# Performance work log

Measured on AMD Instinct MI355X. Metric: run time of the kernel, lower is better.

Reference implementation:

```python
import jax, jax.numpy as jnp
import numpy as np

IN_C = 256
OUT_C = 256
KS = 3
PAD = 1
EPS = 1e-5
BLOCK_SIZE = 256  # largest power of 2 dividing IN_C
NUM_BLOCKS = IN_C // BLOCK_SIZE


def golay_sequence(n):
    pow2 = 1
    while pow2 < n:
        pow2 *= 2
    a = np.array([1.0], dtype=np.float32)
    b = np.array([1.0], dtype=np.float32)
    while len(a) < pow2:
        a, b = np.concatenate([a, b]), np.concatenate([a, -b])
    return a[:n]


def fwht(x):
    """Unnormalized fast Walsh-Hadamard transform over the last axis (Sylvester order)."""
    base = x.shape[:-1]
    n = x.shape[-1]
    h = 1
    while h < n:
        y = x.reshape(base + (n // (2 * h), 2, h))
        a, c = y[..., 0, :], y[..., 1, :]
        x = jnp.stack([a + c, a - c], axis=-2).reshape(base + (n,))
        h *= 2
    return x


def setup_inputs() -> dict:
    key = jax.random.key(0)
    k1, k2, k3 = jax.random.split(key, 3)
    x = jax.random.normal(k1, (32, IN_C, 56, 56), dtype=jnp.float32)
    fan_in = IN_C * KS * KS
    W = jax.random.normal(k2, (OUT_C, IN_C, KS, KS), dtype=jnp.float32) / np.sqrt(fan_in)
    b = jax.random.normal(k3, (OUT_C,), dtype=jnp.float32) * 0.01
    rms_w = jnp.ones((IN_C,), dtype=jnp.float32)
    return {"x": x, "W": W, "b": b, "rms_w": rms_w}


def reference(x, W, b, rms_w):
    n, c, h, w = x.shape
    golay = jnp.asarray(golay_sequence(c)).reshape(1, c, 1, 1)
    x = x * golay                                    # Golay elementwise multiply
    x = jnp.transpose(x, (0, 2, 3, 1))               # NCHW -> NHWC
    x = x.reshape(n, h, w, NUM_BLOCKS, BLOCK_SIZE)
    x = fwht(x)                                      # blockwise Hadamard butterfly
    x = x.reshape(n, h, w, c)
    # RMSNorm over channel dim
    x = x * jax.lax.rsqrt(jnp.mean(x * x, axis=-1, keepdims=True) + EPS) * rms_w
    x = jnp.transpose(x, (0, 3, 1, 2))               # NHWC -> NCHW
    out = jax.lax.conv_general_dilated(
        x, W, window_strides=(1, 1), padding=((PAD, PAD), (PAD, PAD)),
        dimension_numbers=("NCHW", "OIHW", "NCHW"))
    return out + b[None, :, None, None]
```

## Files before the change

kernel.cpp:

```cpp
#include <hip/hip_runtime.h>
#include <hip/hip_bf16.h>

typedef short v8s __attribute__((ext_vector_type(8)));
typedef float v4f __attribute__((ext_vector_type(4)));
typedef float v16f __attribute__((ext_vector_type(16)));
typedef unsigned short u16;

#define PROW 58
#define PCOL 64

static constexpr size_t A_CC_STRIDE = (size_t)32 * PROW * PCOL * 32;
static constexpr size_t A_BYTES     = 8 * A_CC_STRIDE * 2;
static constexpr size_t WB_ELEMS    = (size_t)9 * 8 * 256 * 32;

__device__ __forceinline__ void gl2lds16(const void* gptr, void* lptr) {
  auto g = (const __attribute__((address_space(1))) unsigned int*)gptr;
  auto l = (__attribute__((address_space(3))) unsigned int*)lptr;
  __builtin_amdgcn_global_load_lds(g, l, 16, 0, 0);
}

__device__ __forceinline__ u16 f2bf(float f) {
  __hip_bfloat16 h = __float2bfloat16(f);
  union { __hip_bfloat16 b; u16 u; } cv; cv.b = h; return cv.u;
}

#define WAITVM(K) asm volatile("s_waitcnt vmcnt(" #K ")" ::: "memory")

struct alignas(16) HgTab {
  u16 v[16 * 8 * 64 * 8];
  constexpr HgTab() : v{} {
    for (int ks = 0; ks < 16; ks++)
      for (int nt = 0; nt < 8; nt++)
        for (int l = 0; l < 64; l++)
          for (int j = 0; j < 8; j++) {
            int c  = ks * 16 + ((l >> 5) << 3) + j;
            int cp = (nt << 5) + (l & 31);
            int s  = (__builtin_popcount((unsigned)(c & cp)) +
                      __builtin_popcount((unsigned)(c & (c >> 1)))) & 1;
            v[(((ks << 3) + nt) << 9) + (l << 3) + j] = (u16)(s ? 0xBF80 : 0x3F80);
          }
  }
};
static_assert(sizeof(HgTab) == 131072, "HgTab size");
__device__ const HgTab HG{};

__global__ __launch_bounds__(256, 4) void fwht_kernel(
    const float* __restrict__ x, const float* __restrict__ rms_w,
    u16* __restrict__ A)
{
  __shared__ __align__(16) float xs4[4][16][64];
  __shared__ float ssbuf[2][64];

  const int tid = threadIdx.x;
  const int y = blockIdx.x;
  const int n = blockIdx.y;

  const int lane = tid & 63;
  const int wv   = tid >> 6;
  const int mt   = wv & 1;
  const int nh   = wv >> 1;
  const int l31  = lane & 31;
  const int h    = lane >> 5;

  const int pos  = mt * 32 + l31;
  const int posl = pos > 55 ? 55 : pos;

  const float* xrow = x + (size_t)n * 802816 + (size_t)y * 56;
  const int rr4 = lane >> 4;
  int c4 = (lane & 15) * 4; if (c4 > 52) c4 = 52;

#define FSTG(KS) gl2lds16(xrow + (size_t)((KS) * 16 + wv * 4 + rr4) * 3136 + c4, \
                          &xs4[(KS) & 3][wv * 4 + rr4][(lane & 15) * 4])

  v8s bfr[2][4];
#define LOADB(KS, BK) { _Pragma("unroll") for (int nt = 0; nt < 4; nt++) \
    bfr[BK][nt] = *(const v8s*)(HG.v + ((size_t)((((KS) * 8) + nh * 4 + nt) * 64 + lane)) * 8); }

  v16f acc[4];
  #pragma unroll
  for (int nt = 0; nt < 4; nt++)
    #pragma unroll
    for (int e = 0; e < 16; e++)
      acc[nt][e] = 0.0f;

  FSTG(0);
  LOADB(0, 0)
  FSTG(1);
  FSTG(2);

#define FCOMP(S) { const float* cb = &xs4[(S) & 3][0][0]; v8s ah, al; \
    _Pragma("unroll") for (int j = 0; j < 8; j++) { \
      float v = cb[(h * 8 + j) * 64 + posl]; \
      unsigned u = __float_as_uint(v); \
      unsigned hu = u & 0xFFFF0000u; \
      float r = v - __uint_as_float(hu); \
      ah[j] = (short)(hu >> 16); \
      al[j] = (short)f2bf(r); } \
    _Pragma("unroll") for (int nt = 0; nt < 4; nt++) { \
      acc[nt] = __builtin_amdgcn_mfma_f32_32x32x16_bf16(ah, bfr[(S) & 1][nt], acc[nt], 0, 0, 0); \
      acc[nt] = __builtin_amdgcn_mfma_f32_32x32x16_bf16(al, bfr[(S) & 1][nt], acc[nt], 0, 0, 0); } }

#define FSTEP(S, KV) { \
    if ((S) < 15) LOADB((S) + 1, ((S) + 1) & 1) \
    __builtin_amdgcn_sched_barrier(0); \
    WAITVM(KV); \
    __builtin_amdgcn_sched_barrier(0); \
    __builtin_amdgcn_s_barrier(); \
    if ((S) + 3 <= 15) { FSTG((S) + 3); } \
    __builtin_amdgcn_sched_barrier(0); \
    FCOMP(S) }

  FSTEP(0, 6)  FSTEP(1, 5)  FSTEP(2, 5)  FSTEP(3, 5)
  FSTEP(4, 5)  FSTEP(5, 5)  FSTEP(6, 5)  FSTEP(7, 5)
  FSTEP(8, 5)  FSTEP(9, 5)  FSTEP(10, 5) FSTEP(11, 5)
  FSTEP(12, 5) FSTEP(13, 5) FSTEP(14, 4) FSTEP(15, 0)

  #pragma unroll
  for (int g = 0; g < 16; g++) {
    float s = acc[0][g] * acc[0][g] + acc[1][g] * acc[1][g]
            + acc[2][g] * acc[2][g] + acc[3][g] * acc[3][g];
    #pragma unroll
    for (int m = 1; m <= 16; m <<= 1) s += __shfl_xor(s, m, 64);
    if (l31 == 0)
      ssbuf[nh][mt * 32 + (g & 3) + 8 * (g >> 2) + 4 * h] = s;
  }
  __syncthreads();

  float rwv[4];
  #pragma unroll
  for (int nt = 0; nt < 4; nt++)
    rwv[nt] = rms_w[nh * 128 + nt * 32 + l31];

  const int jj  = lane & 7;
  const int icq = l31 >> 3;

  #pragma unroll
  for (int g = 0; g < 16; g++) {
    const int rg   = (g & 3) + 8 * (g >> 2) + 4 * h;
    const int posg = mt * 32 + rg;
    float ssum = ssbuf[0][posg] + ssbuf[1][posg];
    float sc = rsqrtf(ssum * (1.0f / 256.0f) + 1e-5f);
    if (posg < 56) {
      const int col = posg + 1;
      const size_t rowoff = ((size_t)icq * 64 + col) * 8 + jj;
      #pragma unroll
      for (int nt = 0; nt < 4; nt++) {
        const int cc = nh * 4 + nt;
        size_t go = (((size_t)cc * 32 + n) * PROW + (y + 1)) * 2048 + rowoff;
        A[go] = f2bf(acc[nt][g] * sc * rwv[nt]);
      }
    }
  }

  {
    const v8s z = {0,0,0,0,0,0,0,0};
    int cc = tid >> 5;
    int s  = tid & 31;
    int q  = s >> 3, cidx = s & 7;
    int col = (cidx == 0) ? 0 : (56 + cidx);
    size_t rb = (((size_t)cc * 32 + n) * PROW + (y + 1)) * 2048;
    *(v8s*)(A + rb + ((size_t)q * 64 + col) * 8) = z;
  }
  if (y == 0 || y == 55) {
    const v8s z = {0,0,0,0,0,0,0,0};
    const int r = (y == 0) ? 0 : 57;
    #pragma unroll
    for (int i = 0; i < 8; i++) {
      int c = tid + 256 * i;
      int cc = c >> 8, rem = c & 255;
      size_t go = (((size_t)cc * 32 + n) * PROW + r) * 2048 + rem * 8;
      *(v8s*)(A + go) = z;
    }
  }
#undef FSTG
#undef LOADB
#undef FCOMP
#undef FSTEP
}

__global__ __launch_bounds__(256) void wconv_kernel(
    const float* __restrict__ Wf, u16* __restrict__ Wb)
{
  int t = blockIdx.x * 256 + threadIdx.x;
  int kk = t >> 16;
  int cc = (t >> 13) & 7;
  int r  = t & 8191;
  int ocb = r >> 12;
  int q   = (r >> 10) & 3;
  int ocl = (r >> 3) & 127;
  int j   = r & 7;
  int oc = ocb * 128 + ocl;
  int ic = cc * 32 + q * 8 + j;
  int ky = kk / 3, kx = kk - ky * 3;
  float w = Wf[((oc * 256 + ic) * 3 + ky) * 3 + kx];
  Wb[t] = f2bf(w);
}

__global__ __launch_bounds__(256, 4) void conv_kernel(
    const u16* __restrict__ A, const u16* __restrict__ Wb,
    const float* __restrict__ bias, float* __restrict__ out)
{
  __shared__ __align__(16) u16 As2[2][8192];

  const int tid  = threadIdx.x;
  const int lane = tid & 63;
  const int wv   = tid >> 6;
  const int wm   = wv & 1;
  const int wn   = wv >> 1;
  const int m31  = lane & 31;
  const int kh8  = lane >> 5;

  const int ocb = blockIdx.x;
  const int y0  = blockIdx.y * 2;
  const int n   = blockIdx.z;

  const u16* gA = A + ((size_t)n * PROW + y0) * 2048;

  v16f acc[2][2];
  #pragma unroll
  for (int i = 0; i < 2; i++)
    #pragma unroll
    for (int j = 0; j < 2; j++)
      #pragma unroll
      for (int e = 0; e < 16; e++)
        acc[i][j][e] = 0.0f;

  int ub[2][2];
  #pragma unroll
  for (int nf = 0; nf < 2; nf++)
    #pragma unroll
    for (int kh = 0; kh < 2; kh++) {
      int ocl = wn * 64 + nf * 32 + m31;
      int q = kh * 2 + kh8;
      ub[nf][kh] = (q * 128 + ocl) * 8;
    }

#define STAGE_A(CCV) { const u16* g = gA + (size_t)(CCV) * A_CC_STRIDE + tid * 8; \
    u16* d = &As2[(CCV) & 1][0] + tid * 8; \
    _Pragma("unroll") for (int k = 0; k < 4; k++) gl2lds16(g + k * 2048, d + k * 2048); }

#define CONV_CC(CC) { \
    WAITVM(0); \
    __builtin_amdgcn_s_barrier(); \
    if ((CC) < 7) STAGE_A((CC) + 1) \
    __builtin_amdgcn_sched_barrier(0); \
    { const u16* asb = &As2[(CC) & 1][0]; \
      _Pragma("unroll") for (int ky = 0; ky < 3; ky++) \
        _Pragma("unroll") for (int kx = 0; kx < 3; kx++) { \
          const u16* bt = Wb + (size_t)((((ky * 3 + kx) * 8 + (CC)) * 8192) + ocb * 4096); \
          v8s bf[2][2]; \
          _Pragma("unroll") for (int nf = 0; nf < 2; nf++) \
            _Pragma("unroll") for (int kh = 0; kh < 2; kh++) \
              bf[nf][kh] = *(const v8s*)(bt + ub[nf][kh]); \
          v8s af[2][2]; \
          _Pragma("unroll") for (int mf = 0; mf < 2; mf++) \
            _Pragma("unroll") for (int kh = 0; kh < 2; kh++) { \
              int col = mf * 32 + m31 + kx; \
              col = col > 63 ? 63 : col; \
              int q = kh * 2 + kh8; \
              af[mf][kh] = *(const v8s*)(asb + ((wm + ky) * 4 + q) * 512 + col * 8); } \
          _Pragma("unroll") for (int mf = 0; mf < 2; mf++) \
            _Pragma("unroll") for (int nf = 0; nf < 2; nf++) { \
              acc[mf][nf] = __builtin_amdgcn_mfma_f32_32x32x16_bf16(af[mf][0], bf[nf][0], acc[mf][nf], 0, 0, 0); \
              acc[mf][nf] = __builtin_amdgcn_mfma_f32_32x32x16_bf16(af[mf][1], bf[nf][1], acc[mf][nf], 0, 0, 0); } \
        } } }

  STAGE_A(0)

  CONV_CC(0) CONV_CC(1) CONV_CC(2) CONV_CC(3)
  CONV_CC(4) CONV_CC(5) CONV_CC(6) CONV_CC(7)

#undef STAGE_A
#undef CONV_CC

  const int yrow = y0 + wm;
  #pragma unroll
  for (int nf = 0; nf < 2; nf++) {
    const int oc = ocb * 128 + wn * 64 + nf * 32 + m31;
    const float bb = bias[oc];
    float* orow = out + ((size_t)(n * 256 + oc) * 56 + yrow) * 56;
    #pragma unroll
    for (int mf = 0; mf < 2; mf++) {
      #pragma unroll
      for (int g = 0; g < 4; g++) {
        const int x0 = mf * 32 + 8 * g + 4 * kh8;
        if (x0 < 56) {
          v4f val = { acc[mf][nf][4*g+0] + bb, acc[mf][nf][4*g+1] + bb,
                      acc[mf][nf][4*g+2] + bb, acc[mf][nf][4*g+3] + bb };
          *(v4f*)(orow + x0) = val;
        }
      }
    }
  }
}

extern "C" void kernel_launch(void* const* d_in, const int* in_sizes, int n_in,
                              void* d_out, int out_size, void* d_ws, size_t ws_size,
                              hipStream_t stream)
{
  const float* x     = (const float*)d_in[0];
  const float* Wf    = (const float*)d_in[1];
  const float* bias  = (const float*)d_in[2];
  const float* rms_w = (const float*)d_in[3];
  float* out = (float*)d_out;

  if (ws_size < A_BYTES + WB_ELEMS * 2) return;

  u16* Abf = (u16*)d_ws;
  u16* Wb  = (u16*)((char*)d_ws + A_BYTES);

  fwht_kernel<<<dim3(56, 32), 256, 0, stream>>>(x, rms_w, Abf);
  wconv_kernel<<<dim3((int)(WB_ELEMS / 256)), 256, 0, stream>>>(Wf, Wb);
  conv_kernel<<<dim3(2, 28, 32), 256, 0, stream>>>(Abf, Wb, bias, out);
}
```

Before: 333.1 us.

## Software-pipeline weight fragment loads across ky rows and swizzle block order

Weight (B) fragments for each ky row are now prefetched into registers, in a ping-pong buffer, one ky step ahead, including the next channel chunk's first row. This hides global-load latency behind the MFMAs instead of stalling on each load. The vmcnt wait is relaxed from 0 to 12 so these loads can stay in flight. The grid is flattened to 1D and swizzled so the two output-channel blocks of nearby row pairs run together, which should improve L2 reuse of activations. The larger register footprint forces launch bounds down from 4 to 3 waves, risking lower occupancy.

```diff
diff --git a/kernel.cpp b/kernel.cpp
--- a/kernel.cpp
+++ b/kernel.cpp
@@ -196,7 +196,7 @@
   Wb[t] = f2bf(w);
 }
 
-__global__ __launch_bounds__(256, 4) void conv_kernel(
+__global__ __launch_bounds__(256, 3) void conv_kernel(
     const u16* __restrict__ A, const u16* __restrict__ Wb,
     const float* __restrict__ bias, float* __restrict__ out)
 {
@@ -210,9 +210,13 @@
   const int m31  = lane & 31;
   const int kh8  = lane >> 5;
 
-  const int ocb = blockIdx.x;
-  const int y0  = blockIdx.y * 2;
-  const int n   = blockIdx.z;
+  const int bid = blockIdx.x;
+  const int sg  = bid & 15;
+  const int ocb = sg >> 3;
+  const int pr  = (bid >> 4) * 8 + (sg & 7);
+  const int n   = pr / 28;
+  const int yq  = pr - n * 28;
+  const int y0  = yq * 2;
 
   const u16* gA = A + ((size_t)n * PROW + y0) * 2048;
 
@@ -235,42 +239,56 @@
       ub[nf][kh] = (q * 128 + ocl) * 8;
     }
 
+  v8s bkA[3][2][2], bkB[3][2][2];
+
 #define STAGE_A(CCV) { const u16* g = gA + (size_t)(CCV) * A_CC_STRIDE + tid * 8; \
     u16* d = &As2[(CCV) & 1][0] + tid * 8; \
     _Pragma("unroll") for (int k = 0; k < 4; k++) gl2lds16(g + k * 2048, d + k * 2048); }
 
-#define CONV_CC(CC) { \
-    WAITVM(0); \
+#define LOADBK(DST, CCV, KYV) { _Pragma("unroll") for (int kx = 0; kx < 3; kx++) { \
+    const u16* bt = Wb + (size_t)(((((KYV) * 3 + kx) * 8 + (CCV)) * 8192) + ocb * 4096); \
+    _Pragma("unroll") for (int nf = 0; nf < 2; nf++) \
+      _Pragma("unroll") for (int kh = 0; kh < 2; kh++) \
+        DST[kx][nf][kh] = *(const v8s*)(bt + ub[nf][kh]); } }
+
+#define KYBLK(CC, KY, BUSE) { \
+    const u16* asb = &As2[(CC) & 1][0]; \
+    _Pragma("unroll") for (int kx = 0; kx < 3; kx++) { \
+      v8s af[2][2]; \
+      _Pragma("unroll") for (int mf = 0; mf < 2; mf++) \
+        _Pragma("unroll") for (int kh = 0; kh < 2; kh++) { \
+          int col = mf * 32 + m31 + kx; \
+          col = col > 63 ? 63 : col; \
+          int q = kh * 2 + kh8; \
+          af[mf][kh] = *(const v8s*)(asb + ((wm + (KY)) * 4 + q) * 512 + col * 8); } \
+      _Pragma("unroll") for (int mf = 0; mf < 2; mf++) \
+        _Pragma("unroll") for (int nf = 0; nf < 2; nf++) { \
+          acc[mf][nf] = __builtin_amdgcn_mfma_f32_32x32x16_bf16(af[mf][0], BUSE[kx][nf][0], acc[mf][nf], 0, 0, 0); \
+          acc[mf][nf] = __builtin_amdgcn_mfma_f32_32x32x16_bf16(af[mf][1], BUSE[kx][nf][1], acc[mf][nf], 0, 0, 0); } } }
+
+#define CONV_CC(CC, P, Q) { \
+    WAITVM(12); \
     __builtin_amdgcn_s_barrier(); \
     if ((CC) < 7) STAGE_A((CC) + 1) \
     __builtin_amdgcn_sched_barrier(0); \
-    { const u16* asb = &As2[(CC) & 1][0]; \
-      _Pragma("unroll") for (int ky = 0; ky < 3; ky++) \
-        _Pragma("unroll") for (int kx = 0; kx < 3; kx++) { \
-          const u16* bt = Wb + (size_t)((((ky * 3 + kx) * 8 + (CC)) * 8192) + ocb * 4096); \
-          v8s bf[2][2]; \
-          _Pragma("unroll") for (int nf = 0; nf < 2; nf++) \
-            _Pragma("unroll") for (int kh = 0; kh < 2; kh++) \
-              bf[nf][kh] = *(const v8s*)(bt + ub[nf][kh]); \
-          v8s af[2][2]; \
-          _Pragma("unroll") for (int mf = 0; mf < 2; mf++) \
-            _Pragma("unroll") for (int kh = 0; kh < 2; kh++) { \
-              int col = mf * 32 + m31 + kx; \
-              col = col > 63 ? 63 : col; \
-              int q = kh * 2 + kh8; \
-              af[mf][kh] = *(const v8s*)(asb + ((wm + ky) * 4 + q) * 512 + col * 8); } \
-          _Pragma("unroll") for (int mf = 0; mf < 2; mf++) \
-            _Pragma("unroll") for (int nf = 0; nf < 2; nf++) { \
-              acc[mf][nf] = __builtin_amdgcn_mfma_f32_32x32x16_bf16(af[mf][0], bf[nf][0], acc[mf][nf], 0, 0, 0); \
-              acc[mf][nf] = __builtin_amdgcn_mfma_f32_32x32x16_bf16(af[mf][1], bf[nf][1], acc[mf][nf], 0, 0, 0); } \
-        } } }
+    LOADBK(Q, CC, 1) \
+    KYBLK(CC, 0, P) \
+    LOADBK(P, CC, 2) \
+    KYBLK(CC, 1, Q) \
+    if ((CC) < 7) LOADBK(Q, (CC) + 1, 0) \
+    KYBLK(CC, 2, P) }
 
   STAGE_A(0)
-
-  CONV_CC(0) CONV_CC(1) CONV_CC(2) CONV_CC(3)
-  CONV_CC(4) CONV_CC(5) CONV_CC(6) CONV_CC(7)
+  LOADBK(bkA, 0, 0)
+
+  CONV_CC(0, bkA, bkB) CONV_CC(1, bkB, bkA)
+  CONV_CC(2, bkA, bkB) CONV_CC(3, bkB, bkA)
+  CONV_CC(4, bkA, bkB) CONV_CC(5, bkB, bkA)
+  CONV_CC(6, bkA, bkB) CONV_CC(7, bkB, bkA)
 
 #undef STAGE_A
+#undef LOADBK
+#undef KYBLK
 #undef CONV_CC
 
   const int yrow = y0 + wm;
@@ -311,5 +329,5 @@
 
   fwht_kernel<<<dim3(56, 32), 256, 0, stream>>>(x, rms_w, Abf);
   wconv_kernel<<<dim3((int)(WB_ELEMS / 256)), 256, 0, stream>>>(Wf, Wb);
-  conv_kernel<<<dim3(2, 28, 32), 256, 0, stream>>>(Abf, Wb, bias, out);
-}
+  conv_kernel<<<dim3(1792), 256, 0, stream>>>(Abf, Wb, bias, out);
+}
```

Result: no change. 331.8 us (-0.4%).
